# Kernel optimization log

Measured on AMD Instinct MI355X. Metric: run time of the kernel, lower is better.

## Reference

```python
import jax, jax.numpy as jnp
import numpy as np
from jax import lax

NEG = -jnp.inf


def _lse(x):
    # safe logsumexp over last axis: rows of all -inf give -inf with zero grads
    m = lax.stop_gradient(jnp.max(x, axis=-1, keepdims=True))
    m = jnp.where(jnp.isfinite(m), m, 0.0)
    s = jnp.sum(jnp.exp(x - m), axis=-1)
    return jnp.where(s > 0, jnp.log(jnp.where(s > 0, s, 1.0)), NEG) + m[..., 0]


def _inside(s_arc, s_sib, mask):
    # s_arc[b, dep, head]; s_sib[b, dep, head, sib]; mask[b, s] (col 0 False)
    B, S, _ = s_arc.shape
    A = jnp.transpose(s_arc, (0, 2, 1))        # [b, head, dep]
    SB = jnp.transpose(s_sib, (0, 2, 1, 3))    # [b, head, dep, sib]
    lens = jnp.sum(mask.astype(jnp.int32), axis=1)
    k = jnp.arange(S)[:, None]   # span start index (stripe row)
    j = jnp.arange(S)[None, :]   # offset within stripe (split/sibling)
    d = jnp.arange(S)
    s_i0 = jnp.full((B, S, S), NEG, dtype=s_arc.dtype)  # incomplete spans [b, head, dep]
    s_s0 = s_i0                                          # sibling spans
    s_c0 = s_i0.at[:, d, d].set(0.0)                     # complete spans, width-0 = 0

    def step(carry, w):
        s_i, s_s, s_c = carry
        valid = (k < S - w) & (j < w)
        kw, kj, kj1 = k + w, k + j, k + j + 1
        # left incomplete: I(k+w -> k), siblings at k+1+j
        il = s_i[:, kw, kj1] + s_s[:, kj1, k] + SB[:, kw, k, kj1]
        il = jnp.where(valid, il, NEG)
        il0 = jnp.where(k == 0, 0.0, s_c[:, kw, kw] + s_c[:, k, kw - 1])  # [B,S,1]
        il = jnp.where(j == w - 1, il0, il)
        s_i = jnp.where(k - j == w, _lse(il)[:, None, :] + A, s_i)
        # right incomplete: I(k -> k+w), siblings at k+j (row k=0 forbidden)
        ir = s_i[:, k, kj] + s_s[:, kj, kw] + SB[:, k, kw, kj]
        ir = jnp.where(valid & (k > 0), ir, NEG)
        ir0 = s_c[:, k, k] + s_c[:, kw, k + 1]
        ir = jnp.where(j == 0, ir0, ir)
        s_i = jnp.where(j - k == w, _lse(ir)[:, :, None] + A, s_i)
        # sibling spans S(k, k+w)
        slr = jnp.where(valid, s_c[:, k, kj] + s_c[:, kw, kj1], NEG)
        sl = _lse(slr)
        s_s = jnp.where(k - j == w, sl[:, None, :], s_s)
        s_s = jnp.where(j - k == w, sl[:, :, None], s_s)
        # complete spans (use s_i updated at this width)
        cl = jnp.where(valid, s_c[:, kj, k] + s_i[:, kw, kj], NEG)
        cr = jnp.where(valid, s_i[:, k, kj1] + s_c[:, kj1, kw], NEG)
        s_c = jnp.where(k - j == w, _lse(cl)[:, None, :], s_c)
        s_c = jnp.where(j - k == w, _lse(cr)[:, :, None], s_c)
        # single-root constraint: kill C(0 -> w) for sentences of length != w
        row0 = jnp.where((d[None, :] == w) & (lens[:, None] != w), NEG, s_c[:, 0, :])
        s_c = s_c.at[:, 0, :].set(row0)
        return (s_i, s_s, s_c), None

    (_, _, s_c), _ = lax.scan(jax.checkpoint(step), (s_i0, s_s0, s_c0), jnp.arange(1, S))
    logZ = jnp.take_along_axis(s_c[:, 0, :], lens[:, None], axis=1).sum()
    return logZ


def setup_inputs() -> dict:
    B, S = 16, 128
    key = jax.random.key(0)
    k1, k2, k3, k4 = jax.random.split(key, 4)
    s_arc = jax.random.normal(k1, (B, S, S), jnp.float32)
    s_sib = jax.random.normal(k2, (B, S, S, S), jnp.float32)
    mask = jnp.ones((B, S), bool).at[:, 0].set(False)
    arcs = jax.random.randint(k3, (B, S), 0, S, jnp.int32)
    sibs = jax.random.randint(k4, (B, S, S), 0, S, jnp.int32)
    return {"s_arc": s_arc, "s_sib": s_sib, "mask": mask, "arcs": arcs, "sibs": sibs}


def reference(s_arc, s_sib, mask, arcs, sibs):
    logZ = _inside(s_arc, s_sib, mask)
    arc_sel = jnp.take_along_axis(s_arc, arcs[:, :, None], axis=-1)[..., 0]
    score = jnp.where(mask, arc_sel, 0.0).sum()
    sib_sel = jnp.take_along_axis(s_sib, sibs[..., None], axis=-1)[..., 0]
    score = score + jnp.where(sibs > 0, sib_sel, 0.0).sum()
    loss = (logZ - score) / mask.sum()
    return loss
```

## Files before the change

kernel.cpp:

```cpp
#include <hip/hip_runtime.h>

#define S 128
#define NEGF (-1e30f)
#define MAXB 16
#define NT 1024
#define PKB2 2080000

__device__ float g_ssw[MAXB * S * S];
__device__ float g_spk2[(size_t)MAXB * PKB2];
__device__ float g_logZ[MAXB];
__device__ float g_partials[512];

__device__ __forceinline__ bool mask_at(const unsigned char* m, int i, bool by) {
  return by ? (m[i] != 0) : (((const int*)m)[i] != 0);
}

__device__ __forceinline__ void upd(float& m, float& s, float v) {
  float mn = fmaxf(m, v);
  s = s * __expf(m - mn) + __expf(v - mn);
  m = mn;
}
__device__ __forceinline__ void fold(float& m0, float& s0, float m1, float s1) {
  float mn = fmaxf(m0, m1);
  s0 = s0 * __expf(m0 - mn) + s1 * __expf(m1 - mn);
  m0 = mn;
}
template <int CTRL>
__device__ __forceinline__ float dpp_f(float x) {
  int i = __float_as_int(x);
  return __int_as_float(__builtin_amdgcn_update_dpp(i, i, CTRL, 0xF, 0xF, false));
}
__device__ __forceinline__ void xfold(float& m, float& s, int lp) {
  if (lp >= 1) { float mo = dpp_f<0xB1>(m),  so = dpp_f<0xB1>(s);  fold(m, s, mo, so); }
  if (lp >= 2) { float mo = dpp_f<0x4E>(m),  so = dpp_f<0x4E>(s);  fold(m, s, mo, so); }
  if (lp >= 3) { float mo = dpp_f<0x141>(m), so = dpp_f<0x141>(s); fold(m, s, mo, so); }
  if (lp >= 4) { float mo = dpp_f<0x140>(m), so = dpp_f<0x140>(s); fold(m, s, mo, so); }
}
__device__ __forceinline__ int lp_cap(int cap) {
  return cap >= 16 ? 4 : cap >= 8 ? 3 : cap >= 4 ? 2 : cap >= 2 ? 1 : 0;
}

template <int SA, int SB>
__device__ __forceinline__ void acc2(const float* a, const float* b,
                                     int n, float& M, float& Ss) {
  int i = 0;
  for (; i + 8 <= n; i += 8) {
    float v0 = a[0 * SA] + b[0 * SB];
    float v1 = a[1 * SA] + b[1 * SB];
    float v2 = a[2 * SA] + b[2 * SB];
    float v3 = a[3 * SA] + b[3 * SB];
    float v4 = a[4 * SA] + b[4 * SB];
    float v5 = a[5 * SA] + b[5 * SB];
    float v6 = a[6 * SA] + b[6 * SB];
    float v7 = a[7 * SA] + b[7 * SB];
    float mc = fmaxf(fmaxf(fmaxf(v0, v1), fmaxf(v2, v3)),
                     fmaxf(fmaxf(v4, v5), fmaxf(v6, v7)));
    float s8 = ((__expf(v0 - mc) + __expf(v1 - mc)) +
                (__expf(v2 - mc) + __expf(v3 - mc))) +
               ((__expf(v4 - mc) + __expf(v5 - mc)) +
                (__expf(v6 - mc) + __expf(v7 - mc)));
    float mn = fmaxf(M, mc);
    Ss = Ss * __expf(M - mn) + s8 * __expf(mc - mn);
    M = mn;
    a += 8 * SA; b += 8 * SB;
  }
  for (; i < n; ++i) { upd(M, Ss, a[0] + b[0]); a += SA; b += SB; }
}
template <int SA, int SB, int SC_>
__device__ __forceinline__ void acc3(const float* a, const float* b,
                                     const float* c, int n, float& M, float& Ss) {
  int i = 0;
  for (; i + 8 <= n; i += 8) {
    float v0 = a[0 * SA] + b[0 * SB] + c[0 * SC_];
    float v1 = a[1 * SA] + b[1 * SB] + c[1 * SC_];
    float v2 = a[2 * SA] + b[2 * SB] + c[2 * SC_];
    float v3 = a[3 * SA] + b[3 * SB] + c[3 * SC_];
    float v4 = a[4 * SA] + b[4 * SB] + c[4 * SC_];
    float v5 = a[5 * SA] + b[5 * SB] + c[5 * SC_];
    float v6 = a[6 * SA] + b[6 * SB] + c[6 * SC_];
    float v7 = a[7 * SA] + b[7 * SB] + c[7 * SC_];
    float mc = fmaxf(fmaxf(fmaxf(v0, v1), fmaxf(v2, v3)),
                     fmaxf(fmaxf(v4, v5), fmaxf(v6, v7)));
    float s8 = ((__expf(v0 - mc) + __expf(v1 - mc)) +
                (__expf(v2 - mc) + __expf(v3 - mc))) +
               ((__expf(v4 - mc) + __expf(v5 - mc)) +
                (__expf(v6 - mc) + __expf(v7 - mc)));
    float mn = fmaxf(M, mc);
    Ss = Ss * __expf(M - mn) + s8 * __expf(mc - mn);
    M = mn;
    a += 8 * SA; b += 8 * SB; c += 8 * SC_;
  }
  for (; i < n; ++i) { upd(M, Ss, a[0] + b[0] + c[0]); a += SA; b += SB; c += SC_; }
}

__global__ __launch_bounds__(256) void pack_kernel(const float* __restrict__ sib) {
  const int wn = 2 + (blockIdx.x % 126);
  const int b = blockIdx.x / 126;
  const int nk2 = S - wn;
  const int R = nk2 - 1;
  if (R <= 0) return;
  const int I = wn - 1;
  const float* SBraw = sib + (size_t)b * S * S * S;
  float* dst0 = g_spk2 + (size_t)b * PKB2 + (size_t)128 * (wn - 1) * (wn - 2);
  __shared__ float tile[32][33];
  const int tx = threadIdx.x & 31, ty = threadIdx.x >> 5;
  for (int typ = 0; typ < 2; ++typ) {
    float* dst = dst0 + (size_t)typ * I * 128;
    for (int bi = 0; bi < I; bi += 32) {
      for (int bk = 0; bk < R; bk += 32) {
        for (int yy = ty; yy < 32; yy += 8) {
          int kk = bk + yy, i = bi + tx;
          if (kk < R && i < I) {
            int k = kk + 1, kw2 = k + wn;
            size_t srow = (typ == 0) ? ((size_t)(kw2 * S + k) * S)
                                     : ((size_t)(k * S + kw2) * S);
            tile[yy][tx] = SBraw[srow + (k + 1 + i)];
          }
        }
        __syncthreads();
        for (int yy = ty; yy < 32; yy += 8) {
          int i = bi + yy, kk = bk + tx;
          if (i < I && kk < R) dst[(size_t)i * 128 + kk] = tile[tx][yy];
        }
        __syncthreads();
      }
    }
  }
}

__global__ __launch_bounds__(NT) void dp_kernel(
    const float* __restrict__ arc,
    const unsigned char* __restrict__ mask)
{
  __shared__ float si[S][S];
  __shared__ float sc[S][S];
  __shared__ int len_sh, cnt0_sh;

  const int b = blockIdx.x;
  const int tid = threadIdx.x;
  const float* arc_b = arc + (size_t)b * S * S;
  const float* spk_b = g_spk2 + (size_t)b * PKB2;
  float* ssw = g_ssw + (size_t)b * S * S;

  if (tid == 0) { len_sh = 0; cnt0_sh = 0; }
  __syncthreads();
  if (tid < S && mask[tid] != 0) atomicAdd(&cnt0_sh, 1);
  for (int i = tid; i < S * S; i += NT) {
    (&si[0][0])[i] = NEGF;
    (&sc[0][0])[i] = NEGF;
  }
  __syncthreads();
  const bool bytes = (cnt0_sh >= 64);
  if (tid < S) {
    sc[tid][tid] = 0.0f;
    if (mask_at(mask, b * S + tid, bytes)) atomicAdd(&len_sh, 1);
  }
  __syncthreads();
  const int len = min(len_sh, S - 1);
  if (tid == 0) g_logZ[b] = 0.0f;

  float mP = NEGF, sP = 0.f, arcvP = 0.f;
  if (tid >= 512) {
    const int fam = (tid >= 768);
    const int floc = tid & 255;
    const int lp = lp_cap(256 / (S - 1));
    const int k = floc >> lp;
    if (k < S - 1)
      arcvP = fam ? arc_b[k * S + (k + 1)] : arc_b[(k + 1) * S + k];
  }

  for (int w = 1; w < S; ++w) {
    const int nk = S - w;
    const int wn = w + 1;

    if (tid < 512) {
      const int lp = lp_cap(512 / nk);
      const int p = 1 << lp;
      const int q = tid & (p - 1);
      const int k = tid >> lp;
      if (k >= 1 && k < nk) {
        const int kw = k + w;
        const int ch = w >> lp;
        const int i0 = q * ch;
        const int n = ((q == p - 1) ? w : i0 + ch) - i0;
        float M = NEGF, Ss = 0.f;
        acc2<1, 1>(&sc[k][k] + i0, &sc[kw][k + 1] + i0, n, M, Ss);
        xfold(M, Ss, lp);
        if (q == 0) ssw[w * S + k] = __logf(Ss) + M;
      }
    } else {
      const int fam = (tid >= 768);
      const int floc = tid & 255;
      const int lp = lp_cap(256 / nk);
      const int p = 1 << lp;
      const int q = floc & (p - 1);
      const int k = floc >> lp;
      if (k < nk) {
        const int kw = k + w;
        float bm;
        if (fam == 0) bm = sc[k][k] + sc[kw][k + 1];
        else bm = (k == 0) ? 0.0f : (sc[kw][kw] + sc[k][kw - 1]);
        float m = mP, s = sP;
        if (q == 0) fold(m, s, bm, 1.0f);
        xfold(m, s, lp);
        if (q == 0) {
          const float r = __logf(s) + m + arcvP;
          if (fam == 0) si[k][kw] = r;
          else          si[kw][k] = r;
        }
      }
    }
    __syncthreads();

    if (tid < 512) {
      const int fam = (tid >= 256);
      const int floc = tid & 255;
      const int lp = lp_cap(256 / nk);
      const int p = 1 << lp;
      const int q = floc & (p - 1);
      const int k = floc >> lp;
      if (k < nk) {
        const int kw = k + w;
        const int ch = w >> lp;
        const int i0 = q * ch;
        const int n = ((q == p - 1) ? w : i0 + ch) - i0;
        float M = NEGF, Ss = 0.f;
        if (fam == 0) {
          acc2<S, 1>(&sc[k + i0][k], &si[kw][k] + i0, n, M, Ss);
          xfold(M, Ss, lp);
          if (q == 0) sc[kw][k] = __logf(Ss) + M;
        } else {
          acc2<1, S>(&si[k][k + 1] + i0, &sc[k + 1 + i0][kw], n, M, Ss);
          xfold(M, Ss, lp);
          if (q == 0) {
            const float r = __logf(Ss) + M;
            if (k == 0) {
              if (w == len) g_logZ[b] = r;
              sc[0][w] = (w == len) ? r : NEGF;
            } else {
              sc[k][kw] = r;
            }
          }
        }
      }
    } else {
      mP = NEGF; sP = 0.f; arcvP = 0.f;
      if (wn < S) {
        const int fam = (tid >= 768);
        const int floc = tid & 255;
        const int nk2 = S - wn;
        const int lp = lp_cap(256 / nk2);
        const int p = 1 << lp;
        const int q = floc & (p - 1);
        const int k = floc >> lp;
        if (k < nk2) {
          const int kw2 = k + wn;
          arcvP = (fam == 0) ? arc_b[kw2 * S + k] : arc_b[k * S + kw2];
          if (k >= 1) {
            const int n1n = wn - 1;
            const float* pk = spk_b + (size_t)128 * (wn - 1) * (wn - 2)
                              + (size_t)fam * n1n * 128 + (k - 1);
            const int ch = n1n >> lp;
            const int i0 = q * ch;
            const int n = ((q == p - 1) ? n1n : i0 + ch) - i0;
            if (fam == 0) {
              acc3<1, 1 - S, 128>(&si[k][k + 1] + i0,
                                  ssw + (wn - 1) * S + (k + 1) + i0 * (1 - S),
                                  pk + (size_t)i0 * 128, n, mP, sP);
            } else {
              acc3<1, S, 128>(&si[kw2][k + 1] + i0,
                              ssw + S + k + i0 * S,
                              pk + (size_t)i0 * 128, n, mP, sP);
            }
          }
        }
      }
    }
    __syncthreads();
  }
}

__global__ __launch_bounds__(256) void score_kernel(
    const float* __restrict__ arc, const float* __restrict__ sib,
    const unsigned char* __restrict__ mask, const int* __restrict__ arcs,
    const int* __restrict__ sibs, int B)
{
  __shared__ bool bytes_sh;
  if (threadIdx.x == 0) {
    int c = 0;
    for (int i = 0; i < S; ++i) c += (mask[i] != 0);
    bytes_sh = (c >= 64);
  }
  __syncthreads();
  const bool bytes = bytes_sh;

  const int total = B * S * S;
  int tid = blockIdx.x * blockDim.x + threadIdx.x;
  float sum = 0.f, cnt = 0.f;
  for (int e = tid; e < total; e += gridDim.x * blockDim.x) {
    int sv = sibs[e];
    if (sv > 0) sum += sib[(size_t)e * S + sv];
    if ((e & (S - 1)) == 0) {
      int bi = e >> 7;
      if (mask_at(mask, bi, bytes)) { sum += arc[(size_t)bi * S + arcs[bi]]; cnt += 1.f; }
    }
  }
  __shared__ float rs[256], rc[256];
  rs[threadIdx.x] = sum; rc[threadIdx.x] = cnt;
  __syncthreads();
  for (int off = 128; off; off >>= 1) {
    if (threadIdx.x < off) {
      rs[threadIdx.x] += rs[threadIdx.x + off];
      rc[threadIdx.x] += rc[threadIdx.x + off];
    }
    __syncthreads();
  }
  if (threadIdx.x == 0) {
    g_partials[blockIdx.x * 2]     = rs[0];
    g_partials[blockIdx.x * 2 + 1] = rc[0];
  }
}

__global__ __launch_bounds__(256) void final_kernel(int B, float* __restrict__ out)
{
  __shared__ float rs[256], rc[256];
  int t = threadIdx.x;
  float v = -g_partials[t * 2];
  float c = g_partials[t * 2 + 1];
  if (t < B) v += g_logZ[t];
  rs[t] = v; rc[t] = c;
  __syncthreads();
  for (int off = 128; off; off >>= 1) {
    if (t < off) { rs[t] += rs[t + off]; rc[t] += rc[t + off]; }
    __syncthreads();
  }
  if (t == 0) out[0] = rs[0] / rc[0];
}

extern "C" void kernel_launch(void* const* d_in, const int* in_sizes, int n_in,
                              void* d_out, int out_size, void* d_ws, size_t ws_size,
                              hipStream_t stream) {
  const float* s_arc = (const float*)d_in[0];
  const float* s_sib = (const float*)d_in[1];
  const unsigned char* mask = (const unsigned char*)d_in[2];
  const int* arcs = (const int*)d_in[3];
  const int* sibs = (const int*)d_in[4];
  int B = in_sizes[0] / (S * S);
  if (B > MAXB) B = MAXB;

  pack_kernel<<<dim3(B * 126), dim3(256), 0, stream>>>(s_sib);
  score_kernel<<<dim3(256), dim3(256), 0, stream>>>(s_arc, s_sib, mask, arcs, sibs, B);
  dp_kernel<<<dim3(B), dim3(NT), 0, stream>>>(s_arc, mask);
  final_kernel<<<dim3(1), dim3(256), 0, stream>>>(B, (float*)d_out);
}
```

Baseline: 619.3 us.

## Stage packed sibling scores into LDS via async global-to-LDS loads

The pack kernel now lays out sibling scores as contiguous per-row segments with odd padded row length instead of a transposed 128-stride layout. Each DP step issues global_load_lds copies of the next width's packed segment into a shared staging buffer, and the accumulation then reads sibling scores from LDS with unit stride. This is meant to cut strided global-memory latency in the serial DP loop and shrink the packed buffer. The risks are extra LDS pressure (about 32KB more), which may limit occupancy, and the need to order the async LDS writes against the barrier before they are read.

```diff
diff --git a/kernel.cpp b/kernel.cpp
--- a/kernel.cpp
+++ b/kernel.cpp
@@ -4,15 +4,22 @@
 #define NEGF (-1e30f)
 #define MAXB 16
 #define NT 1024
-#define PKB2 2080000
+#define STAGE_SZ 8064
+#define PKB 700000
 
 __device__ float g_ssw[MAXB * S * S];
-__device__ float g_spk2[(size_t)MAXB * PKB2];
+__device__ float g_spk[(size_t)MAXB * PKB];
 __device__ float g_logZ[MAXB];
 __device__ float g_partials[512];
 
 __device__ __forceinline__ bool mask_at(const unsigned char* m, int i, bool by) {
   return by ? (m[i] != 0) : (((const int*)m)[i] != 0);
+}
+
+__device__ __forceinline__ void gload_lds4(const float* g, float* l) {
+  __builtin_amdgcn_global_load_lds(
+      (const __attribute__((address_space(1))) unsigned int*)g,
+      (__attribute__((address_space(3))) unsigned int*)l, 4, 0, 0);
 }
 
 __device__ __forceinline__ void upd(float& m, float& s, float v) {
@@ -97,34 +104,26 @@
   const int wn = 2 + (blockIdx.x % 126);
   const int b = blockIdx.x / 126;
   const int nk2 = S - wn;
-  const int R = nk2 - 1;
-  if (R <= 0) return;
-  const int I = wn - 1;
+  const int rows1 = nk2 - 1;
+  if (rows1 <= 0) return;
+  const int rowlen = wn - 1;
+  const int rlP = rowlen | 1;
+  int off = 0;
+  for (int v = 2; v < wn; ++v) off += 2 * (S - v - 1) * ((v - 1) | 1);
   const float* SBraw = sib + (size_t)b * S * S * S;
-  float* dst0 = g_spk2 + (size_t)b * PKB2 + (size_t)128 * (wn - 1) * (wn - 2);
-  __shared__ float tile[32][33];
-  const int tx = threadIdx.x & 31, ty = threadIdx.x >> 5;
-  for (int typ = 0; typ < 2; ++typ) {
-    float* dst = dst0 + (size_t)typ * I * 128;
-    for (int bi = 0; bi < I; bi += 32) {
-      for (int bk = 0; bk < R; bk += 32) {
-        for (int yy = ty; yy < 32; yy += 8) {
-          int kk = bk + yy, i = bi + tx;
-          if (kk < R && i < I) {
-            int k = kk + 1, kw2 = k + wn;
-            size_t srow = (typ == 0) ? ((size_t)(kw2 * S + k) * S)
-                                     : ((size_t)(k * S + kw2) * S);
-            tile[yy][tx] = SBraw[srow + (k + 1 + i)];
-          }
-        }
-        __syncthreads();
-        for (int yy = ty; yy < 32; yy += 8) {
-          int i = bi + yy, kk = bk + tx;
-          if (i < I && kk < R) dst[(size_t)i * 128 + kk] = tile[tx][yy];
-        }
-        __syncthreads();
-      }
-    }
+  float* dst = g_spk + (size_t)b * PKB + off;
+  const int lane5 = threadIdx.x & 31;
+  const int R = 2 * rows1;
+  for (int r = (threadIdx.x >> 5); r < R; r += 8) {
+    const int typ = (r >= rows1) ? 1 : 0;
+    const int kr = (r - typ * rows1) + 1;
+    const int kw2 = kr + wn;
+    const size_t srcoff = (typ == 0)
+        ? ((size_t)(kw2 * S + kr) * S + (kr + 1))
+        : ((size_t)(kr * S + kw2) * S + (kr + 1));
+    const float* src = SBraw + srcoff;
+    float* d = dst + r * rlP;
+    for (int i = lane5; i < rowlen; i += 32) d[i] = src[i];
   }
 }
 
@@ -134,12 +133,13 @@
 {
   __shared__ float si[S][S];
   __shared__ float sc[S][S];
+  __shared__ float stage[STAGE_SZ];
   __shared__ int len_sh, cnt0_sh;
 
   const int b = blockIdx.x;
   const int tid = threadIdx.x;
   const float* arc_b = arc + (size_t)b * S * S;
-  const float* spk_b = g_spk2 + (size_t)b * PKB2;
+  const float* spk_b = g_spk + (size_t)b * PKB;
   float* ssw = g_ssw + (size_t)b * S * S;
 
   if (tid == 0) { len_sh = 0; cnt0_sh = 0; }
@@ -169,9 +169,23 @@
       arcvP = fam ? arc_b[k * S + (k + 1)] : arc_b[(k + 1) * S + k];
   }
 
+  int spk_off = 0;
+
   for (int w = 1; w < S; ++w) {
     const int nk = S - w;
     const int wn = w + 1;
+
+    if (wn < S) {
+      const int rows1n = S - wn - 1;
+      const int T = 2 * rows1n * ((wn - 1) | 1);
+      const float* src = spk_b + spk_off;
+      const int wv = tid >> 6, l = tid & 63;
+      for (int c = wv; c * 64 < T; c += 16) {
+        const int e = c * 64 + l;
+        if (e < T) gload_lds4(src + e, &stage[c * 64]);
+      }
+      spk_off += T;
+    }
 
     if (tid < 512) {
       const int lp = lp_cap(512 / nk);
@@ -258,19 +272,18 @@
           arcvP = (fam == 0) ? arc_b[kw2 * S + k] : arc_b[k * S + kw2];
           if (k >= 1) {
             const int n1n = wn - 1;
-            const float* pk = spk_b + (size_t)128 * (wn - 1) * (wn - 2)
-                              + (size_t)fam * n1n * 128 + (k - 1);
+            const int rlPn = n1n | 1;
             const int ch = n1n >> lp;
             const int i0 = q * ch;
             const int n = ((q == p - 1) ? n1n : i0 + ch) - i0;
             if (fam == 0) {
-              acc3<1, 1 - S, 128>(&si[k][k + 1] + i0,
-                                  ssw + (wn - 1) * S + (k + 1) + i0 * (1 - S),
-                                  pk + (size_t)i0 * 128, n, mP, sP);
+              acc3<1, 1 - S, 1>(&si[k][k + 1] + i0,
+                                ssw + (wn - 1) * S + (k + 1) + i0 * (1 - S),
+                                &stage[(k - 1) * rlPn] + i0, n, mP, sP);
             } else {
-              acc3<1, S, 128>(&si[kw2][k + 1] + i0,
-                              ssw + S + k + i0 * S,
-                              pk + (size_t)i0 * 128, n, mP, sP);
+              acc3<1, S, 1>(&si[kw2][k + 1] + i0,
+                            ssw + S + k + i0 * S,
+                            &stage[((nk2 - 1) + (k - 1)) * rlPn] + i0, n, mP, sP);
             }
           }
         }
```

After: 537.9 us. -13.1%, faster.
